# Performance work log

Measured on AMD Instinct MI355X. Metric: run time of the kernel, lower is better.

## Reference

```python
import jax, jax.numpy as jnp
import numpy as np

DRUG_DIM, PROT_DIM, HIDDEN_DIM, OUTPUT_DIM = 128, 128, 256, 256


def setup_inputs() -> dict:
    key = jax.random.key(0)
    ks = jax.random.split(key, 7)
    B, n_d, n_p = 8, 64, 1024
    s = lambda d: 1.0 / np.sqrt(d)
    return {
        "X_d": jax.random.normal(ks[0], (B, n_d, DRUG_DIM), dtype=jnp.float32),
        "X_p": jax.random.normal(ks[1], (B, n_p, PROT_DIM), dtype=jnp.float32),
        # nn.Linear(in, out) weights have shape (out, in); we store transposed (in, out)
        "W_d": jax.random.uniform(ks[2], (DRUG_DIM, HIDDEN_DIM), jnp.float32, -s(DRUG_DIM), s(DRUG_DIM)),
        "W_p": jax.random.uniform(ks[3], (PROT_DIM, HIDDEN_DIM), jnp.float32, -s(PROT_DIM), s(PROT_DIM)),
        "W_a": jax.random.uniform(ks[4], (DRUG_DIM, OUTPUT_DIM), jnp.float32, -s(DRUG_DIM), s(DRUG_DIM)),
        "W_b": jax.random.uniform(ks[5], (PROT_DIM, OUTPUT_DIM), jnp.float32, -s(PROT_DIM), s(PROT_DIM)),
        "w_score": jax.random.uniform(ks[6], (HIDDEN_DIM,), jnp.float32, -s(HIDDEN_DIM), s(HIDDEN_DIM)),
    }


def reference(X_d, X_p, W_d, W_p, W_a, W_b, w_score):
    # Projections: (B, n_d, H), (B, n_p, H), (B, n_d, O), (B, n_p, O)
    hd = jnp.einsum("bik,kh->bih", X_d, W_d)
    hp = jnp.einsum("bjk,kh->bjh", X_p, W_p)
    fd = jnp.einsum("bik,ko->bio", X_d, W_a)
    fp = jnp.einsum("bjk,ko->bjo", X_p, W_b)

    # N_ij = tanh(hd_i + hp_j): (B, n_d, n_p, H); scores = N @ w_score
    N = jnp.tanh(hd[:, :, None, :] + hp[:, None, :, :])
    scores = jnp.einsum("bijh,h->bij", N, w_score)
    A = jax.nn.softmax(scores, axis=-1)  # softmax over protein dim

    # f_ij = tanh(fd_i + fp_j): (B, n_d, n_p, O)
    f = jnp.tanh(fd[:, :, None, :] + fp[:, None, :, :])
    X_int = jnp.einsum("bij,bijo->bo", A, f)  # sum over i and j
    return X_int
```

## Files before the change

### kernel.cpp

```cpp
#include <hip/hip_runtime.h>

#define NB   8
#define ND   64
#define NP   1024
#define KDIM 128
#define HID  256
#define OUTD 256
#define CSC  2.885390081777927f
#define PSTR 1048

typedef __attribute__((ext_vector_type(8))) short  bf16x8;
typedef __attribute__((ext_vector_type(4))) float  f32x4;


__device__ __forceinline__ ushort f2bf(float f) {
    unsigned u = __float_as_uint(f);
    return (ushort)((u + 0x7FFFu + ((u >> 16) & 1u)) >> 16);
}

__device__ __forceinline__ float comb4(float u1, float u2, float u3, float u4,
                                       float c1, float c2, float c3, float c4,
                                       float acc) {
    float p12 = u1 * u2, p34 = u3 * u4;
    float P   = p12 * p34;
    float t1  = fmaf(c1, u2, c2 * u1);
    float t2  = fmaf(c3, u4, c4 * u3);
    float num = fmaf(t1, p34, t2 * p12);
    return fmaf(num, __builtin_amdgcn_rcpf(P), acc);
}

__global__ __launch_bounds__(256) void k_cast(
    const float* __restrict__ Xd, const float* __restrict__ Xp,
    const float* __restrict__ Wd, const float* __restrict__ Wa,
    const float* __restrict__ Wp, const float* __restrict__ Wb,
    ushort* __restrict__ Xdbf, ushort* __restrict__ Xpbf,
    ushort* __restrict__ WdT, ushort* __restrict__ WaT,
    ushort* __restrict__ WpT, ushort* __restrict__ WbT) {
    int blk = blockIdx.x, t = threadIdx.x;
    if (blk < 1024) {
        size_t i = ((size_t)blk << 10) + ((size_t)t << 2);
        float4 v = *(const float4*)(Xp + i);
        ushort4 o; o.x = f2bf(v.x); o.y = f2bf(v.y); o.z = f2bf(v.z); o.w = f2bf(v.w);
        *(ushort4*)(Xpbf + i) = o;
    } else if (blk < 1088) {
        size_t i = ((size_t)(blk - 1024) << 10) + ((size_t)t << 2);
        float4 v = *(const float4*)(Xd + i);
        ushort4 o; o.x = f2bf(v.x); o.y = f2bf(v.y); o.z = f2bf(v.z); o.w = f2bf(v.w);
        *(ushort4*)(Xdbf + i) = o;
    } else {
        int r = blk - 1088, mat = r >> 5;
        const float* W = (mat == 0) ? Wd : (mat == 1) ? Wa : (mat == 2) ? Wp : Wb;
        ushort* WT = (mat == 0) ? WdT : (mat == 1) ? WaT : (mat == 2) ? WpT : WbT;
        int o0 = ((r & 31) << 10) + (t << 2);
        int n = o0 >> 7, k0 = o0 & 127;
        ushort4 o;
        o.x = f2bf(W[(k0 + 0) * HID + n]);
        o.y = f2bf(W[(k0 + 1) * HID + n]);
        o.z = f2bf(W[(k0 + 2) * HID + n]);
        o.w = f2bf(W[(k0 + 3) * HID + n]);
        *(ushort4*)(WT + o0) = o;
    }
}

__global__ __launch_bounds__(256) void k_proj_mfma(
    const ushort* __restrict__ Xpbf, const ushort* __restrict__ Xdbf,
    const ushort* __restrict__ WdT, const ushort* __restrict__ WaT,
    const ushort* __restrict__ WpT, const ushort* __restrict__ WbT,
    float* __restrict__ Ehd, float* __restrict__ Efd,
    float* __restrict__ EhpT, float* __restrict__ Efp) {
    int blk = blockIdx.x, t = threadIdx.x;
    const ushort *A, *B;
    float* out; size_t obase; int ostride, am0, bn0;
    if (blk < 512) {
        int mt = blk >> 2, nt = blk & 3;
        A = Xpbf; am0 = mt * 64; B = WbT; bn0 = nt * 64;
        out = Efp; obase = (size_t)am0 * HID + bn0; ostride = HID;
    } else if (blk < 1024) {
        int r = blk - 512, b = r >> 6, rr = r & 63;
        int mt = rr >> 4, nt = rr & 15;
        A = WpT; am0 = mt * 64;
        B = Xpbf + (size_t)b * NP * KDIM; bn0 = nt * 64;
        out = EhpT; obase = ((size_t)(b * 256 + am0)) * NP + bn0; ostride = NP;
    } else if (blk < 1056) {
        int r = blk - 1024; int mt = r >> 2, nt = r & 3;
        A = Xdbf; am0 = mt * 64; B = WdT; bn0 = nt * 64;
        out = Ehd; obase = (size_t)am0 * HID + bn0; ostride = HID;
    } else {
        int r = blk - 1056; int mt = r >> 2, nt = r & 3;
        A = Xdbf; am0 = mt * 64; B = WaT; bn0 = nt * 64;
        out = Efd; obase = (size_t)am0 * HID + bn0; ostride = HID;
    }
    int l = t & 63, w = t >> 6;
    int wm = (w >> 1) << 5, wn = (w & 1) << 5;
    int lr = l & 15, lk = (l >> 4) << 3;
    const ushort* Ab = A + (size_t)(am0 + wm + lr) * KDIM + lk;
    const ushort* Bb = B + (size_t)(bn0 + wn + lr) * KDIM + lk;

    bf16x8 af[2][4], bfr[2][4];
#pragma unroll
    for (int f = 0; f < 2; ++f)
#pragma unroll
        for (int ks = 0; ks < 4; ++ks) {
            af[f][ks]  = *(const bf16x8*)(Ab + (size_t)(f << 4) * KDIM + (ks << 5));
            bfr[f][ks] = *(const bf16x8*)(Bb + (size_t)(f << 4) * KDIM + (ks << 5));
        }

    f32x4 acc[2][2];
#pragma unroll
    for (int mf = 0; mf < 2; ++mf)
#pragma unroll
        for (int nf = 0; nf < 2; ++nf) acc[mf][nf] = (f32x4){0.f, 0.f, 0.f, 0.f};
#pragma unroll
    for (int ks = 0; ks < 4; ++ks)
#pragma unroll
        for (int mf = 0; mf < 2; ++mf)
#pragma unroll
            for (int nf = 0; nf < 2; ++nf)
                acc[mf][nf] = __builtin_amdgcn_mfma_f32_16x16x32_bf16(
                    af[mf][ks], bfr[nf][ks], acc[mf][nf], 0, 0, 0);

#pragma unroll
    for (int mf = 0; mf < 2; ++mf)
#pragma unroll
        for (int nf = 0; nf < 2; ++nf)
#pragma unroll
            for (int r = 0; r < 4; ++r) {
                int m = wm + (mf << 4) + ((l >> 4) << 2) + r;
                int n = wn + (nf << 4) + (l & 15);
                out[obase + (size_t)m * ostride + n] =
                    __builtin_amdgcn_exp2f(acc[mf][nf][r] * CSC);
            }
}

__global__ __launch_bounds__(1024, 4) void k_fused(
    const float* __restrict__ Ehd, const float* __restrict__ EhpT,
    const float* __restrict__ Efd, const float* __restrict__ Efp,
    const float* __restrict__ wsc, float* __restrict__ part) {
    int blk = blockIdx.x;
    int b = blk & 7, pair = blk >> 3;
    int row0 = b * ND + pair * 2;
    int t = threadIdx.x;

    __shared__ float2 hrow[256];
    __shared__ float  w2s[256];
    __shared__ float2 a2[1024];
    __shared__ float  sred[8 * PSTR];
    __shared__ float  wsum0[16], wsum1[16];

    if (t < 256) {
        hrow[t] = make_float2(Ehd[((size_t)row0 << 8) + t],
                              Ehd[((size_t)(row0 + 1) << 8) + t]);
        w2s[t] = -2.0f * wsc[t];
    }
    __syncthreads();

    {
        int jq = t & 255, hq = t >> 8;
        const float* pB = EhpT + ((size_t)((b << 8) + (hq << 6))) * NP + (jq << 2);
        float a00 = 0, a01 = 0, a02 = 0, a03 = 0;
        float a10 = 0, a11 = 0, a12 = 0, a13 = 0;
        for (int hg = 0; hg < 16; ++hg) {
            const float* pr = pB + (size_t)(hg << 2) * NP;
            float4 p0 = *(const float4*)(pr);
            float4 p1 = *(const float4*)(pr + NP);
            float4 p2 = *(const float4*)(pr + 2 * (size_t)NP);
            float4 p3 = *(const float4*)(pr + 3 * (size_t)NP);
            int h = (hq << 6) + (hg << 2);
            float2 h0 = hrow[h],     h1 = hrow[h + 1];
            float2 h2 = hrow[h + 2], h3 = hrow[h + 3];
            float w0 = w2s[h],     w1 = w2s[h + 1];
            float w2 = w2s[h + 2], w3 = w2s[h + 3];
            a00 = comb4(fmaf(h0.x, p0.x, 1.f), fmaf(h1.x, p1.x, 1.f),
                        fmaf(h2.x, p2.x, 1.f), fmaf(h3.x, p3.x, 1.f),
                        w0, w1, w2, w3, a00);
            a01 = comb4(fmaf(h0.x, p0.y, 1.f), fmaf(h1.x, p1.y, 1.f),
                        fmaf(h2.x, p2.y, 1.f), fmaf(h3.x, p3.y, 1.f),
                        w0, w1, w2, w3, a01);
            a02 = comb4(fmaf(h0.x, p0.z, 1.f), fmaf(h1.x, p1.z, 1.f),
                        fmaf(h2.x, p2.z, 1.f), fmaf(h3.x, p3.z, 1.f),
                        w0, w1, w2, w3, a02);
            a03 = comb4(fmaf(h0.x, p0.w, 1.f), fmaf(h1.x, p1.w, 1.f),
                        fmaf(h2.x, p2.w, 1.f), fmaf(h3.x, p3.w, 1.f),
                        w0, w1, w2, w3, a03);
            a10 = comb4(fmaf(h0.y, p0.x, 1.f), fmaf(h1.y, p1.x, 1.f),
                        fmaf(h2.y, p2.x, 1.f), fmaf(h3.y, p3.x, 1.f),
                        w0, w1, w2, w3, a10);
            a11 = comb4(fmaf(h0.y, p0.y, 1.f), fmaf(h1.y, p1.y, 1.f),
                        fmaf(h2.y, p2.y, 1.f), fmaf(h3.y, p3.y, 1.f),
                        w0, w1, w2, w3, a11);
            a12 = comb4(fmaf(h0.y, p0.z, 1.f), fmaf(h1.y, p1.z, 1.f),
                        fmaf(h2.y, p2.z, 1.f), fmaf(h3.y, p3.z, 1.f),
                        w0, w1, w2, w3, a12);
            a13 = comb4(fmaf(h0.y, p0.w, 1.f), fmaf(h1.y, p1.w, 1.f),
                        fmaf(h2.y, p2.w, 1.f), fmaf(h3.y, p3.w, 1.f),
                        w0, w1, w2, w3, a13);
        }
        int base = (hq << 8) + jq;
        sred[0 * PSTR + base] = a00;  sred[1 * PSTR + base] = a01;
        sred[2 * PSTR + base] = a02;  sred[3 * PSTR + base] = a03;
        sred[4 * PSTR + base] = a10;  sred[5 * PSTR + base] = a11;
        sred[6 * PSTR + base] = a12;  sred[7 * PSTR + base] = a13;
    }
    __syncthreads();

    {
        int jq2 = t >> 2, c = t & 3;
        const float* p0 = sred + c * PSTR + jq2;
        const float* p1 = sred + (4 + c) * PSTR + jq2;
        float sc0 = (p0[0] + p0[256]) + (p0[512] + p0[768]);
        float sc1 = (p1[0] + p1[256]) + (p1[512] + p1[768]);
        const float L2E = 1.4426950408889634f;
        float e0 = __builtin_amdgcn_exp2f(sc0 * L2E);
        float e1 = __builtin_amdgcn_exp2f(sc1 * L2E);
        float s0 = e0, s1 = e1;
#pragma unroll
        for (int off = 32; off > 0; off >>= 1) {
            s0 += __shfl_xor(s0, off, 64);
            s1 += __shfl_xor(s1, off, 64);
        }
        if ((t & 63) == 0) { wsum0[t >> 6] = s0; wsum1[t >> 6] = s1; }
        __syncthreads();
        float tot0 = 0.f, tot1 = 0.f;
#pragma unroll
        for (int w = 0; w < 16; ++w) { tot0 += wsum0[w]; tot1 += wsum1[w]; }
        float sn0 = -2.0f * __builtin_amdgcn_rcpf(tot0);
        float sn1 = -2.0f * __builtin_amdgcn_rcpf(tot1);
        a2[t] = make_float2(e0 * sn0, e1 * sn1);
    }
    __syncthreads();

    {
        int oq = t & 63, jg = t >> 6;
        int o0 = oq << 2;
        float4 fd0 = *(const float4*)(Efd + ((size_t)row0 << 8) + o0);
        float4 fd1 = *(const float4*)(Efd + ((size_t)(row0 + 1) << 8) + o0);
        const float* fpB = Efp + ((size_t)(b * NP + (jg << 6)) << 8) + o0;
        float b00 = 0, b01 = 0, b02 = 0, b03 = 0;
        float b10 = 0, b11 = 0, b12 = 0, b13 = 0;
        for (int g = 0; g < 16; ++g) {
            const float* fr = fpB + ((size_t)(g << 2) << 8);
            float4 f0 = *(const float4*)(fr);
            float4 f1 = *(const float4*)(fr + 256);
            float4 f2 = *(const float4*)(fr + 512);
            float4 f3 = *(const float4*)(fr + 768);
            int j0 = (jg << 6) + (g << 2);
            float2 A0 = a2[j0],     A1 = a2[j0 + 1];
            float2 A2v = a2[j0 + 2], A3 = a2[j0 + 3];
            b00 = comb4(fmaf(fd0.x, f0.x, 1.f), fmaf(fd0.x, f1.x, 1.f),
                        fmaf(fd0.x, f2.x, 1.f), fmaf(fd0.x, f3.x, 1.f),
                        A0.x, A1.x, A2v.x, A3.x, b00);
            b01 = comb4(fmaf(fd0.y, f0.y, 1.f), fmaf(fd0.y, f1.y, 1.f),
                        fmaf(fd0.y, f2.y, 1.f), fmaf(fd0.y, f3.y, 1.f),
                        A0.x, A1.x, A2v.x, A3.x, b01);
            b02 = comb4(fmaf(fd0.z, f0.z, 1.f), fmaf(fd0.z, f1.z, 1.f),
                        fmaf(fd0.z, f2.z, 1.f), fmaf(fd0.z, f3.z, 1.f),
                        A0.x, A1.x, A2v.x, A3.x, b02);
            b03 = comb4(fmaf(fd0.w, f0.w, 1.f), fmaf(fd0.w, f1.w, 1.f),
                        fmaf(fd0.w, f2.w, 1.f), fmaf(fd0.w, f3.w, 1.f),
                        A0.x, A1.x, A2v.x, A3.x, b03);
            b10 = comb4(fmaf(fd1.x, f0.x, 1.f), fmaf(fd1.x, f1.x, 1.f),
                        fmaf(fd1.x, f2.x, 1.f), fmaf(fd1.x, f3.x, 1.f),
                        A0.y, A1.y, A2v.y, A3.y, b10);
            b11 = comb4(fmaf(fd1.y, f0.y, 1.f), fmaf(fd1.y, f1.y, 1.f),
                        fmaf(fd1.y, f2.y, 1.f), fmaf(fd1.y, f3.y, 1.f),
                        A0.y, A1.y, A2v.y, A3.y, b11);
            b12 = comb4(fmaf(fd1.z, f0.z, 1.f), fmaf(fd1.z, f1.z, 1.f),
                        fmaf(fd1.z, f2.z, 1.f), fmaf(fd1.z, f3.z, 1.f),
                        A0.y, A1.y, A2v.y, A3.y, b12);
            b13 = comb4(fmaf(fd1.w, f0.w, 1.f), fmaf(fd1.w, f1.w, 1.f),
                        fmaf(fd1.w, f2.w, 1.f), fmaf(fd1.w, f3.w, 1.f),
                        A0.y, A1.y, A2v.y, A3.y, b13);
        }
        __syncthreads();
        int base = (jg << 6) + oq;
        sred[0 * PSTR + base] = b00;  sred[1 * PSTR + base] = b01;
        sred[2 * PSTR + base] = b02;  sred[3 * PSTR + base] = b03;
        sred[4 * PSTR + base] = b10;  sred[5 * PSTR + base] = b11;
        sred[6 * PSTR + base] = b12;  sred[7 * PSTR + base] = b13;
    }
    __syncthreads();

    if (t < 512) {
        int r = t >> 8, o = t & 255;
        int oq2 = o >> 2, c2 = o & 3;
        const float* pk = sred + (r * 4 + c2) * PSTR + oq2;
        float s = 0.f;
#pragma unroll
        for (int g = 0; g < 16; ++g) s += pk[g << 6];
        part[((size_t)((b << 6) + (pair << 1) + r) << 8) + o] = s;
    }
}

__global__ __launch_bounds__(256) void k_reduce(
    const float* __restrict__ part, float* __restrict__ out) {
    int b = blockIdx.x, t = threadIdx.x;
    float s = 64.0f;
#pragma unroll 8
    for (int i = 0; i < 64; ++i)
        s += part[((size_t)((b << 6) + i) << 8) + t];
    out[(b << 8) + t] = s;
}

extern "C" void kernel_launch(void* const* d_in, const int* in_sizes, int n_in,
                              void* d_out, int out_size, void* d_ws, size_t ws_size,
                              hipStream_t stream) {
    const float* Xd  = (const float*)d_in[0];
    const float* Xp  = (const float*)d_in[1];
    const float* Wd  = (const float*)d_in[2];
    const float* Wp  = (const float*)d_in[3];
    const float* Wa  = (const float*)d_in[4];
    const float* Wb  = (const float*)d_in[5];
    const float* wsc = (const float*)d_in[6];
    float* out = (float*)d_out;

    float* ws = (float*)d_ws;
    float* Ehd  = ws;
    float* Efd  = Ehd + NB * ND * HID;
    float* EhpT = Efd + NB * ND * OUTD;
    float* Efp  = EhpT + NB * NP * HID;
    float* stage = Efp + NB * NP * OUTD;
    ushort* Xpbf = (ushort*)stage;
    ushort* Xdbf = Xpbf + NB * NP * KDIM;
    ushort* WdT  = Xdbf + 65536;
    ushort* WaT  = WdT + 32768;
    ushort* WpT  = WaT + 32768;
    ushort* WbT  = WpT + 32768;
    float* part  = stage;

    k_cast     <<<1216, 256, 0, stream>>>(Xd, Xp, Wd, Wa, Wp, Wb,
                                          Xdbf, Xpbf, WdT, WaT, WpT, WbT);
    k_proj_mfma<<<1088, 256, 0, stream>>>(Xpbf, Xdbf, WdT, WaT, WpT, WbT,
                                          Ehd, Efd, EhpT, Efp);
    k_fused    <<<256, 1024, 0, stream>>>(Ehd, EhpT, Efd, Efp, wsc, part);
    k_reduce   <<<NB, 256, 0, stream>>>(part, out);
}
```

Measured before the change: 59.31 us.

## Split fused attention kernel into scores, softmax, and accumulation kernels

Replaces the single 1024-thread fused kernel (256 blocks) with separate kernels. Scores are computed over quarter protein ranges in 1024 blocks of 256 threads, followed by a row softmax kernel and a 1024-block f-accumulation kernel that writes per-quarter partials. A wider 64-block reduction finishes the sum. The aim is to fill more compute units and shrink per-block shared memory, at the cost of extra launches and round trips of the score matrix through global memory.

```diff
diff --git a/kernel.cpp b/kernel.cpp
--- a/kernel.cpp
+++ b/kernel.cpp
@@ -7,7 +7,7 @@
 #define HID  256
 #define OUTD 256
 #define CSC  2.885390081777927f
-#define PSTR 1048
+#define PSTR2 264
 
 typedef __attribute__((ext_vector_type(8))) short  bf16x8;
 typedef __attribute__((ext_vector_type(4))) float  f32x4;
@@ -132,173 +132,186 @@
             }
 }
 
-__global__ __launch_bounds__(1024, 4) void k_fused(
+__global__ __launch_bounds__(256) void k_scores2(
     const float* __restrict__ Ehd, const float* __restrict__ EhpT,
-    const float* __restrict__ Efd, const float* __restrict__ Efp,
-    const float* __restrict__ wsc, float* __restrict__ part) {
+    const float* __restrict__ wsc, float* __restrict__ S) {
     int blk = blockIdx.x;
-    int b = blk & 7, pair = blk >> 3;
+    int b = blk & 7, pair = (blk >> 3) & 31, jh = blk >> 8;
     int row0 = b * ND + pair * 2;
     int t = threadIdx.x;
-
     __shared__ float2 hrow[256];
     __shared__ float  w2s[256];
-    __shared__ float2 a2[1024];
-    __shared__ float  sred[8 * PSTR];
-    __shared__ float  wsum0[16], wsum1[16];
-
-    if (t < 256) {
-        hrow[t] = make_float2(Ehd[((size_t)row0 << 8) + t],
-                              Ehd[((size_t)(row0 + 1) << 8) + t]);
-        w2s[t] = -2.0f * wsc[t];
-    }
-    __syncthreads();
-
-    {
-        int jq = t & 255, hq = t >> 8;
-        const float* pB = EhpT + ((size_t)((b << 8) + (hq << 6))) * NP + (jq << 2);
-        float a00 = 0, a01 = 0, a02 = 0, a03 = 0;
-        float a10 = 0, a11 = 0, a12 = 0, a13 = 0;
-        for (int hg = 0; hg < 16; ++hg) {
-            const float* pr = pB + (size_t)(hg << 2) * NP;
-            float4 p0 = *(const float4*)(pr);
-            float4 p1 = *(const float4*)(pr + NP);
-            float4 p2 = *(const float4*)(pr + 2 * (size_t)NP);
-            float4 p3 = *(const float4*)(pr + 3 * (size_t)NP);
-            int h = (hq << 6) + (hg << 2);
-            float2 h0 = hrow[h],     h1 = hrow[h + 1];
-            float2 h2 = hrow[h + 2], h3 = hrow[h + 3];
-            float w0 = w2s[h],     w1 = w2s[h + 1];
-            float w2 = w2s[h + 2], w3 = w2s[h + 3];
-            a00 = comb4(fmaf(h0.x, p0.x, 1.f), fmaf(h1.x, p1.x, 1.f),
-                        fmaf(h2.x, p2.x, 1.f), fmaf(h3.x, p3.x, 1.f),
-                        w0, w1, w2, w3, a00);
-            a01 = comb4(fmaf(h0.x, p0.y, 1.f), fmaf(h1.x, p1.y, 1.f),
-                        fmaf(h2.x, p2.y, 1.f), fmaf(h3.x, p3.y, 1.f),
-                        w0, w1, w2, w3, a01);
-            a02 = comb4(fmaf(h0.x, p0.z, 1.f), fmaf(h1.x, p1.z, 1.f),
-                        fmaf(h2.x, p2.z, 1.f), fmaf(h3.x, p3.z, 1.f),
-                        w0, w1, w2, w3, a02);
-            a03 = comb4(fmaf(h0.x, p0.w, 1.f), fmaf(h1.x, p1.w, 1.f),
-                        fmaf(h2.x, p2.w, 1.f), fmaf(h3.x, p3.w, 1.f),
-                        w0, w1, w2, w3, a03);
-            a10 = comb4(fmaf(h0.y, p0.x, 1.f), fmaf(h1.y, p1.x, 1.f),
-                        fmaf(h2.y, p2.x, 1.f), fmaf(h3.y, p3.x, 1.f),
-                        w0, w1, w2, w3, a10);
-            a11 = comb4(fmaf(h0.y, p0.y, 1.f), fmaf(h1.y, p1.y, 1.f),
-                        fmaf(h2.y, p2.y, 1.f), fmaf(h3.y, p3.y, 1.f),
-                        w0, w1, w2, w3, a11);
-            a12 = comb4(fmaf(h0.y, p0.z, 1.f), fmaf(h1.y, p1.z, 1.f),
-                        fmaf(h2.y, p2.z, 1.f), fmaf(h3.y, p3.z, 1.f),
-                        w0, w1, w2, w3, a12);
-            a13 = comb4(fmaf(h0.y, p0.w, 1.f), fmaf(h1.y, p1.w, 1.f),
-                        fmaf(h2.y, p2.w, 1.f), fmaf(h3.y, p3.w, 1.f),
-                        w0, w1, w2, w3, a13);
-        }
-        int base = (hq << 8) + jq;
-        sred[0 * PSTR + base] = a00;  sred[1 * PSTR + base] = a01;
-        sred[2 * PSTR + base] = a02;  sred[3 * PSTR + base] = a03;
-        sred[4 * PSTR + base] = a10;  sred[5 * PSTR + base] = a11;
-        sred[6 * PSTR + base] = a12;  sred[7 * PSTR + base] = a13;
-    }
-    __syncthreads();
-
-    {
-        int jq2 = t >> 2, c = t & 3;
-        const float* p0 = sred + c * PSTR + jq2;
-        const float* p1 = sred + (4 + c) * PSTR + jq2;
-        float sc0 = (p0[0] + p0[256]) + (p0[512] + p0[768]);
-        float sc1 = (p1[0] + p1[256]) + (p1[512] + p1[768]);
-        const float L2E = 1.4426950408889634f;
-        float e0 = __builtin_amdgcn_exp2f(sc0 * L2E);
-        float e1 = __builtin_amdgcn_exp2f(sc1 * L2E);
-        float s0 = e0, s1 = e1;
-#pragma unroll
-        for (int off = 32; off > 0; off >>= 1) {
-            s0 += __shfl_xor(s0, off, 64);
-            s1 += __shfl_xor(s1, off, 64);
-        }
-        if ((t & 63) == 0) { wsum0[t >> 6] = s0; wsum1[t >> 6] = s1; }
+    __shared__ float  sred[8 * PSTR2];
+    hrow[t] = make_float2(Ehd[((size_t)row0 << 8) + t],
+                          Ehd[((size_t)(row0 + 1) << 8) + t]);
+    w2s[t] = -2.0f * wsc[t];
+    __syncthreads();
+
+    int jq = t & 63, hq = t >> 6;
+    const float* pB = EhpT + ((size_t)((b << 8) + (hq << 6))) * NP
+                    + (jh << 8) + (jq << 2);
+    float a00 = 0, a01 = 0, a02 = 0, a03 = 0;
+    float a10 = 0, a11 = 0, a12 = 0, a13 = 0;
+    for (int hg = 0; hg < 16; ++hg) {
+        const float* pr = pB + (size_t)(hg << 2) * NP;
+        float4 p0 = *(const float4*)(pr);
+        float4 p1 = *(const float4*)(pr + NP);
+        float4 p2 = *(const float4*)(pr + 2 * (size_t)NP);
+        float4 p3 = *(const float4*)(pr + 3 * (size_t)NP);
+        int h = (hq << 6) + (hg << 2);
+        float2 h0 = hrow[h],     h1 = hrow[h + 1];
+        float2 h2 = hrow[h + 2], h3 = hrow[h + 3];
+        float w0 = w2s[h],     w1 = w2s[h + 1];
+        float w2 = w2s[h + 2], w3 = w2s[h + 3];
+        a00 = comb4(fmaf(h0.x, p0.x, 1.f), fmaf(h1.x, p1.x, 1.f),
+                    fmaf(h2.x, p2.x, 1.f), fmaf(h3.x, p3.x, 1.f),
+                    w0, w1, w2, w3, a00);
+        a01 = comb4(fmaf(h0.x, p0.y, 1.f), fmaf(h1.x, p1.y, 1.f),
+                    fmaf(h2.x, p2.y, 1.f), fmaf(h3.x, p3.y, 1.f),
+                    w0, w1, w2, w3, a01);
+        a02 = comb4(fmaf(h0.x, p0.z, 1.f), fmaf(h1.x, p1.z, 1.f),
+                    fmaf(h2.x, p2.z, 1.f), fmaf(h3.x, p3.z, 1.f),
+                    w0, w1, w2, w3, a02);
+        a03 = comb4(fmaf(h0.x, p0.w, 1.f), fmaf(h1.x, p1.w, 1.f),
+                    fmaf(h2.x, p2.w, 1.f), fmaf(h3.x, p3.w, 1.f),
+                    w0, w1, w2, w3, a03);
+        a10 = comb4(fmaf(h0.y, p0.x, 1.f), fmaf(h1.y, p1.x, 1.f),
+                    fmaf(h2.y, p2.x, 1.f), fmaf(h3.y, p3.x, 1.f),
+                    w0, w1, w2, w3, a10);
+        a11 = comb4(fmaf(h0.y, p0.y, 1.f), fmaf(h1.y, p1.y, 1.f),
+                    fmaf(h2.y, p2.y, 1.f), fmaf(h3.y, p3.y, 1.f),
+                    w0, w1, w2, w3, a11);
+        a12 = comb4(fmaf(h0.y, p0.z, 1.f), fmaf(h1.y, p1.z, 1.f),
+                    fmaf(h2.y, p2.z, 1.f), fmaf(h3.y, p3.z, 1.f),
+                    w0, w1, w2, w3, a12);
+        a13 = comb4(fmaf(h0.y, p0.w, 1.f), fmaf(h1.y, p1.w, 1.f),
+                    fmaf(h2.y, p2.w, 1.f), fmaf(h3.y, p3.w, 1.f),
+                    w0, w1, w2, w3, a13);
+    }
+    int base = (hq << 6) + jq;
+    sred[0 * PSTR2 + base] = a00;  sred[1 * PSTR2 + base] = a01;
+    sred[2 * PSTR2 + base] = a02;  sred[3 * PSTR2 + base] = a03;
+    sred[4 * PSTR2 + base] = a10;  sred[5 * PSTR2 + base] = a11;
+    sred[6 * PSTR2 + base] = a12;  sred[7 * PSTR2 + base] = a13;
+    __syncthreads();
+
+    int c = t & 3, jq2 = t >> 2;
+    const float* q0 = sred + c * PSTR2 + jq2;
+    const float* q1 = sred + (4 + c) * PSTR2 + jq2;
+    float s0 = (q0[0] + q0[64]) + (q0[128] + q0[192]);
+    float s1 = (q1[0] + q1[64]) + (q1[128] + q1[192]);
+    S[((size_t)row0 << 10) + (jh << 8) + t] = s0;
+    S[((size_t)(row0 + 1) << 10) + (jh << 8) + t] = s1;
+}
+
+__global__ __launch_bounds__(256) void k_softmax(float* __restrict__ S) {
+    int row = blockIdx.x;
+    int t = threadIdx.x;
+    float* Srow = S + ((size_t)row << 10);
+    float4 v = ((float4*)Srow)[t];
+    const float L2E = 1.4426950408889634f;
+    v.x = __builtin_amdgcn_exp2f(v.x * L2E);
+    v.y = __builtin_amdgcn_exp2f(v.y * L2E);
+    v.z = __builtin_amdgcn_exp2f(v.z * L2E);
+    v.w = __builtin_amdgcn_exp2f(v.w * L2E);
+    float s4 = (v.x + v.y) + (v.z + v.w);
+#pragma unroll
+    for (int off = 32; off > 0; off >>= 1) s4 += __shfl_xor(s4, off, 64);
+    __shared__ float wsum[4];
+    if ((t & 63) == 0) wsum[t >> 6] = s4;
+    __syncthreads();
+    float tot = (wsum[0] + wsum[1]) + (wsum[2] + wsum[3]);
+    float sneg = -2.0f * __builtin_amdgcn_rcpf(tot);
+    v.x *= sneg; v.y *= sneg; v.z *= sneg; v.w *= sneg;
+    ((float4*)Srow)[t] = v;
+}
+
+__global__ __launch_bounds__(256) void k_facc2(
+    const float* __restrict__ Efd, const float* __restrict__ Efp,
+    const float* __restrict__ A2, float* __restrict__ npart) {
+    int blk = blockIdx.x;
+    int b = blk & 7, pair = (blk >> 3) & 31, jh = blk >> 8;
+    int row0 = b * ND + pair * 2;
+    int t = threadIdx.x;
+    __shared__ float2 a2s[256];
+    __shared__ float  sred[8 * PSTR2];
+    a2s[t] = make_float2(A2[((size_t)row0 << 10) + (jh << 8) + t],
+                         A2[((size_t)(row0 + 1) << 10) + (jh << 8) + t]);
+    __syncthreads();
+
+    int oq = t & 63, jg = t >> 6;
+    int o0 = oq << 2;
+    float4 fd0 = *(const float4*)(Efd + ((size_t)row0 << 8) + o0);
+    float4 fd1 = *(const float4*)(Efd + ((size_t)(row0 + 1) << 8) + o0);
+    const float* fpB = Efp + ((size_t)(b * NP + (jh << 8) + (jg << 6)) << 8) + o0;
+    float b00 = 0, b01 = 0, b02 = 0, b03 = 0;
+    float b10 = 0, b11 = 0, b12 = 0, b13 = 0;
+    for (int g = 0; g < 16; ++g) {
+        const float* fr = fpB + ((size_t)(g << 2) << 8);
+        float4 f0 = *(const float4*)(fr);
+        float4 f1 = *(const float4*)(fr + 256);
+        float4 f2 = *(const float4*)(fr + 512);
+        float4 f3 = *(const float4*)(fr + 768);
+        int j0 = (jg << 6) + (g << 2);
+        float2 A0 = a2s[j0],      A1 = a2s[j0 + 1];
+        float2 A2v = a2s[j0 + 2], A3 = a2s[j0 + 3];
+        b00 = comb4(fmaf(fd0.x, f0.x, 1.f), fmaf(fd0.x, f1.x, 1.f),
+                    fmaf(fd0.x, f2.x, 1.f), fmaf(fd0.x, f3.x, 1.f),
+                    A0.x, A1.x, A2v.x, A3.x, b00);
+        b01 = comb4(fmaf(fd0.y, f0.y, 1.f), fmaf(fd0.y, f1.y, 1.f),
+                    fmaf(fd0.y, f2.y, 1.f), fmaf(fd0.y, f3.y, 1.f),
+                    A0.x, A1.x, A2v.x, A3.x, b01);
+        b02 = comb4(fmaf(fd0.z, f0.z, 1.f), fmaf(fd0.z, f1.z, 1.f),
+                    fmaf(fd0.z, f2.z, 1.f), fmaf(fd0.z, f3.z, 1.f),
+                    A0.x, A1.x, A2v.x, A3.x, b02);
+        b03 = comb4(fmaf(fd0.w, f0.w, 1.f), fmaf(fd0.w, f1.w, 1.f),
+                    fmaf(fd0.w, f2.w, 1.f), fmaf(fd0.w, f3.w, 1.f),
+                    A0.x, A1.x, A2v.x, A3.x, b03);
+        b10 = comb4(fmaf(fd1.x, f0.x, 1.f), fmaf(fd1.x, f1.x, 1.f),
+                    fmaf(fd1.x, f2.x, 1.f), fmaf(fd1.x, f3.x, 1.f),
+                    A0.y, A1.y, A2v.y, A3.y, b10);
+        b11 = comb4(fmaf(fd1.y, f0.y, 1.f), fmaf(fd1.y, f1.y, 1.f),
+                    fmaf(fd1.y, f2.y, 1.f), fmaf(fd1.y, f3.y, 1.f),
+                    A0.y, A1.y, A2v.y, A3.y, b11);
+        b12 = comb4(fmaf(fd1.z, f0.z, 1.f), fmaf(fd1.z, f1.z, 1.f),
+                    fmaf(fd1.z, f2.z, 1.f), fmaf(fd1.z, f3.z, 1.f),
+                    A0.y, A1.y, A2v.y, A3.y, b12);
+        b13 = comb4(fmaf(fd1.w, f0.w, 1.f), fmaf(fd1.w, f1.w, 1.f),
+                    fmaf(fd1.w, f2.w, 1.f), fmaf(fd1.w, f3.w, 1.f),
+                    A0.y, A1.y, A2v.y, A3.y, b13);
+    }
+    int base = (jg << 6) + oq;
+    sred[0 * PSTR2 + base] = b00;  sred[1 * PSTR2 + base] = b01;
+    sred[2 * PSTR2 + base] = b02;  sred[3 * PSTR2 + base] = b03;
+    sred[4 * PSTR2 + base] = b10;  sred[5 * PSTR2 + base] = b11;
+    sred[6 * PSTR2 + base] = b12;  sred[7 * PSTR2 + base] = b13;
+    __syncthreads();
+
+    int c = t & 3, oq2 = t >> 2;
+    const float* q0 = sred + c * PSTR2 + oq2;
+    const float* q1 = sred + (4 + c) * PSTR2 + oq2;
+    float s0 = (q0[0] + q0[64]) + (q0[128] + q0[192]);
+    float s1 = (q1[0] + q1[64]) + (q1[128] + q1[192]);
+    npart[((((size_t)row0 << 2) + jh) << 8) + t] = s0;
+    npart[((((size_t)(row0 + 1) << 2) + jh) << 8) + t] = s1;
+}
+
+__global__ __launch_bounds__(256) void k_reduce(
+    const float* __restrict__ npart, float* __restrict__ out) {
+    int b = blockIdx.x >> 3, oc = blockIdx.x & 7;
+    int t = threadIdx.x;
+    int o = oc * 32 + (t & 31), q0 = t >> 5;
+    float s = 0.f;
+#pragma unroll
+    for (int k = 0; k < 32; ++k)
+        s += npart[((size_t)(b * 256 + q0 + (k << 3)) << 8) + o];
+    __shared__ float red[256];
+    red[t] = s; __syncthreads();
+    for (int st = 128; st >= 32; st >>= 1) {
+        if (t < st) red[t] += red[t + st];
         __syncthreads();
-        float tot0 = 0.f, tot1 = 0.f;
-#pragma unroll
-        for (int w = 0; w < 16; ++w) { tot0 += wsum0[w]; tot1 += wsum1[w]; }
-        float sn0 = -2.0f * __builtin_amdgcn_rcpf(tot0);
-        float sn1 = -2.0f * __builtin_amdgcn_rcpf(tot1);
-        a2[t] = make_float2(e0 * sn0, e1 * sn1);
-    }
-    __syncthreads();
-
-    {
-        int oq = t & 63, jg = t >> 6;
-        int o0 = oq << 2;
-        float4 fd0 = *(const float4*)(Efd + ((size_t)row0 << 8) + o0);
-        float4 fd1 = *(const float4*)(Efd + ((size_t)(row0 + 1) << 8) + o0);
-        const float* fpB = Efp + ((size_t)(b * NP + (jg << 6)) << 8) + o0;
-        float b00 = 0, b01 = 0, b02 = 0, b03 = 0;
-        float b10 = 0, b11 = 0, b12 = 0, b13 = 0;
-        for (int g = 0; g < 16; ++g) {
-            const float* fr = fpB + ((size_t)(g << 2) << 8);
-            float4 f0 = *(const float4*)(fr);
-            float4 f1 = *(const float4*)(fr + 256);
-            float4 f2 = *(const float4*)(fr + 512);
-            float4 f3 = *(const float4*)(fr + 768);
-            int j0 = (jg << 6) + (g << 2);
-            float2 A0 = a2[j0],     A1 = a2[j0 + 1];
-            float2 A2v = a2[j0 + 2], A3 = a2[j0 + 3];
-            b00 = comb4(fmaf(fd0.x, f0.x, 1.f), fmaf(fd0.x, f1.x, 1.f),
-                        fmaf(fd0.x, f2.x, 1.f), fmaf(fd0.x, f3.x, 1.f),
-                        A0.x, A1.x, A2v.x, A3.x, b00);
-            b01 = comb4(fmaf(fd0.y, f0.y, 1.f), fmaf(fd0.y, f1.y, 1.f),
-                        fmaf(fd0.y, f2.y, 1.f), fmaf(fd0.y, f3.y, 1.f),
-                        A0.x, A1.x, A2v.x, A3.x, b01);
-            b02 = comb4(fmaf(fd0.z, f0.z, 1.f), fmaf(fd0.z, f1.z, 1.f),
-                        fmaf(fd0.z, f2.z, 1.f), fmaf(fd0.z, f3.z, 1.f),
-                        A0.x, A1.x, A2v.x, A3.x, b02);
-            b03 = comb4(fmaf(fd0.w, f0.w, 1.f), fmaf(fd0.w, f1.w, 1.f),
-                        fmaf(fd0.w, f2.w, 1.f), fmaf(fd0.w, f3.w, 1.f),
-                        A0.x, A1.x, A2v.x, A3.x, b03);
-            b10 = comb4(fmaf(fd1.x, f0.x, 1.f), fmaf(fd1.x, f1.x, 1.f),
-                        fmaf(fd1.x, f2.x, 1.f), fmaf(fd1.x, f3.x, 1.f),
-                        A0.y, A1.y, A2v.y, A3.y, b10);
-            b11 = comb4(fmaf(fd1.y, f0.y, 1.f), fmaf(fd1.y, f1.y, 1.f),
-                        fmaf(fd1.y, f2.y, 1.f), fmaf(fd1.y, f3.y, 1.f),
-                        A0.y, A1.y, A2v.y, A3.y, b11);
-            b12 = comb4(fmaf(fd1.z, f0.z, 1.f), fmaf(fd1.z, f1.z, 1.f),
-                        fmaf(fd1.z, f2.z, 1.f), fmaf(fd1.z, f3.z, 1.f),
-                        A0.y, A1.y, A2v.y, A3.y, b12);
-            b13 = comb4(fmaf(fd1.w, f0.w, 1.f), fmaf(fd1.w, f1.w, 1.f),
-                        fmaf(fd1.w, f2.w, 1.f), fmaf(fd1.w, f3.w, 1.f),
-                        A0.y, A1.y, A2v.y, A3.y, b13);
-        }
-        __syncthreads();
-        int base = (jg << 6) + oq;
-        sred[0 * PSTR + base] = b00;  sred[1 * PSTR + base] = b01;
-        sred[2 * PSTR + base] = b02;  sred[3 * PSTR + base] = b03;
-        sred[4 * PSTR + base] = b10;  sred[5 * PSTR + base] = b11;
-        sred[6 * PSTR + base] = b12;  sred[7 * PSTR + base] = b13;
-    }
-    __syncthreads();
-
-    if (t < 512) {
-        int r = t >> 8, o = t & 255;
-        int oq2 = o >> 2, c2 = o & 3;
-        const float* pk = sred + (r * 4 + c2) * PSTR + oq2;
-        float s = 0.f;
-#pragma unroll
-        for (int g = 0; g < 16; ++g) s += pk[g << 6];
-        part[((size_t)((b << 6) + (pair << 1) + r) << 8) + o] = s;
-    }
-}
-
-__global__ __launch_bounds__(256) void k_reduce(
-    const float* __restrict__ part, float* __restrict__ out) {
-    int b = blockIdx.x, t = threadIdx.x;
-    float s = 64.0f;
-#pragma unroll 8
-    for (int i = 0; i < 64; ++i)
-        s += part[((size_t)((b << 6) + i) << 8) + t];
-    out[(b << 8) + t] = s;
+    }
+    if (t < 32) out[(b << 8) + oc * 32 + t] = 64.0f + red[t];
 }
 
 extern "C" void kernel_launch(void* const* d_in, const int* in_sizes, int n_in,
@@ -325,12 +338,15 @@
     ushort* WaT  = WdT + 32768;
     ushort* WpT  = WaT + 32768;
     ushort* WbT  = WpT + 32768;
-    float* part  = stage;
+    float* S     = stage;
+    float* npart = stage + 622592;
 
     k_cast     <<<1216, 256, 0, stream>>>(Xd, Xp, Wd, Wa, Wp, Wb,
                                           Xdbf, Xpbf, WdT, WaT, WpT, WbT);
     k_proj_mfma<<<1088, 256, 0, stream>>>(Xpbf, Xdbf, WdT, WaT, WpT, WbT,
                                           Ehd, Efd, EhpT, Efp);
-    k_fused    <<<256, 1024, 0, stream>>>(Ehd, EhpT, Efd, Efp, wsc, part);
-    k_reduce   <<<NB, 256, 0, stream>>>(part, out);
-}
+    k_scores2  <<<1024, 256, 0, stream>>>(Ehd, EhpT, wsc, S);
+    k_softmax  <<<NB * ND, 256, 0, stream>>>(S);
+    k_facc2    <<<1024, 256, 0, stream>>>(Efd, Efp, S, npart);
+    k_reduce   <<<64, 256, 0, stream>>>(npart, out);
+}
```

Result: slower. 61.81 us (+4.2%).

## Split protein dimension across two blocks with deferred softmax normalization

Applied to the files above, without the earlier changes.

Doubles the k_fused grid by splitting the 1024 protein positions into two halves per drug-row pair. Each block writes an unnormalized numerator and a partial softmax denominator, and k_reduce combines them and divides. This gives 512 blocks instead of 256 to fill more CUs, and hrow/w2s are packed into one float4 shared array. The cost is an extra workspace buffer, a reciprocal per row in the reduce kernel, and exp without max subtraction split across halves.

```diff
diff --git a/kernel.cpp b/kernel.cpp
--- a/kernel.cpp
+++ b/kernel.cpp
@@ -7,7 +7,7 @@
 #define HID  256
 #define OUTD 256
 #define CSC  2.885390081777927f
-#define PSTR 1048
+#define PSTR 1032
 
 typedef __attribute__((ext_vector_type(8))) short  bf16x8;
 typedef __attribute__((ext_vector_type(4))) float  f32x4;
@@ -132,70 +132,68 @@
             }
 }
 
-__global__ __launch_bounds__(1024, 4) void k_fused(
+__global__ __launch_bounds__(1024, 8) void k_fused(
     const float* __restrict__ Ehd, const float* __restrict__ EhpT,
     const float* __restrict__ Efd, const float* __restrict__ Efp,
-    const float* __restrict__ wsc, float* __restrict__ part) {
+    const float* __restrict__ wsc, float* __restrict__ num,
+    float* __restrict__ den) {
     int blk = blockIdx.x;
-    int b = blk & 7, pair = blk >> 3;
+    int b = blk & 7, pair = (blk >> 3) & 31, jh = blk >> 8;
     int row0 = b * ND + pair * 2;
     int t = threadIdx.x;
 
-    __shared__ float2 hrow[256];
-    __shared__ float  w2s[256];
-    __shared__ float2 a2[1024];
+    __shared__ float4 hw4[256];
+    __shared__ float2 a2[512];
     __shared__ float  sred[8 * PSTR];
-    __shared__ float  wsum0[16], wsum1[16];
-
-    if (t < 256) {
-        hrow[t] = make_float2(Ehd[((size_t)row0 << 8) + t],
-                              Ehd[((size_t)(row0 + 1) << 8) + t]);
-        w2s[t] = -2.0f * wsc[t];
-    }
+    __shared__ float  wsum0[8], wsum1[8];
+
+    if (t < 256)
+        hw4[t] = make_float4(Ehd[((size_t)row0 << 8) + t],
+                             Ehd[((size_t)(row0 + 1) << 8) + t],
+                             -2.0f * wsc[t], 0.f);
     __syncthreads();
 
     {
-        int jq = t & 255, hq = t >> 8;
-        const float* pB = EhpT + ((size_t)((b << 8) + (hq << 6))) * NP + (jq << 2);
+        int jq = t & 127, hq = t >> 7;
+        const float* pB = EhpT + ((size_t)((b << 8) + (hq << 5))) * NP
+                        + (jh << 9) + (jq << 2);
         float a00 = 0, a01 = 0, a02 = 0, a03 = 0;
         float a10 = 0, a11 = 0, a12 = 0, a13 = 0;
-        for (int hg = 0; hg < 16; ++hg) {
+        for (int hg = 0; hg < 8; ++hg) {
             const float* pr = pB + (size_t)(hg << 2) * NP;
             float4 p0 = *(const float4*)(pr);
             float4 p1 = *(const float4*)(pr + NP);
             float4 p2 = *(const float4*)(pr + 2 * (size_t)NP);
             float4 p3 = *(const float4*)(pr + 3 * (size_t)NP);
-            int h = (hq << 6) + (hg << 2);
-            float2 h0 = hrow[h],     h1 = hrow[h + 1];
-            float2 h2 = hrow[h + 2], h3 = hrow[h + 3];
-            float w0 = w2s[h],     w1 = w2s[h + 1];
-            float w2 = w2s[h + 2], w3 = w2s[h + 3];
-            a00 = comb4(fmaf(h0.x, p0.x, 1.f), fmaf(h1.x, p1.x, 1.f),
-                        fmaf(h2.x, p2.x, 1.f), fmaf(h3.x, p3.x, 1.f),
-                        w0, w1, w2, w3, a00);
-            a01 = comb4(fmaf(h0.x, p0.y, 1.f), fmaf(h1.x, p1.y, 1.f),
-                        fmaf(h2.x, p2.y, 1.f), fmaf(h3.x, p3.y, 1.f),
-                        w0, w1, w2, w3, a01);
-            a02 = comb4(fmaf(h0.x, p0.z, 1.f), fmaf(h1.x, p1.z, 1.f),
-                        fmaf(h2.x, p2.z, 1.f), fmaf(h3.x, p3.z, 1.f),
-                        w0, w1, w2, w3, a02);
-            a03 = comb4(fmaf(h0.x, p0.w, 1.f), fmaf(h1.x, p1.w, 1.f),
-                        fmaf(h2.x, p2.w, 1.f), fmaf(h3.x, p3.w, 1.f),
-                        w0, w1, w2, w3, a03);
-            a10 = comb4(fmaf(h0.y, p0.x, 1.f), fmaf(h1.y, p1.x, 1.f),
-                        fmaf(h2.y, p2.x, 1.f), fmaf(h3.y, p3.x, 1.f),
-                        w0, w1, w2, w3, a10);
-            a11 = comb4(fmaf(h0.y, p0.y, 1.f), fmaf(h1.y, p1.y, 1.f),
-                        fmaf(h2.y, p2.y, 1.f), fmaf(h3.y, p3.y, 1.f),
-                        w0, w1, w2, w3, a11);
-            a12 = comb4(fmaf(h0.y, p0.z, 1.f), fmaf(h1.y, p1.z, 1.f),
-                        fmaf(h2.y, p2.z, 1.f), fmaf(h3.y, p3.z, 1.f),
-                        w0, w1, w2, w3, a12);
-            a13 = comb4(fmaf(h0.y, p0.w, 1.f), fmaf(h1.y, p1.w, 1.f),
-                        fmaf(h2.y, p2.w, 1.f), fmaf(h3.y, p3.w, 1.f),
-                        w0, w1, w2, w3, a13);
-        }
-        int base = (hq << 8) + jq;
+            int h = (hq << 5) + (hg << 2);
+            float4 hw0 = hw4[h],     hw1 = hw4[h + 1];
+            float4 hw2 = hw4[h + 2], hw3 = hw4[h + 3];
+            a00 = comb4(fmaf(hw0.x, p0.x, 1.f), fmaf(hw1.x, p1.x, 1.f),
+                        fmaf(hw2.x, p2.x, 1.f), fmaf(hw3.x, p3.x, 1.f),
+                        hw0.z, hw1.z, hw2.z, hw3.z, a00);
+            a01 = comb4(fmaf(hw0.x, p0.y, 1.f), fmaf(hw1.x, p1.y, 1.f),
+                        fmaf(hw2.x, p2.y, 1.f), fmaf(hw3.x, p3.y, 1.f),
+                        hw0.z, hw1.z, hw2.z, hw3.z, a01);
+            a02 = comb4(fmaf(hw0.x, p0.z, 1.f), fmaf(hw1.x, p1.z, 1.f),
+                        fmaf(hw2.x, p2.z, 1.f), fmaf(hw3.x, p3.z, 1.f),
+                        hw0.z, hw1.z, hw2.z, hw3.z, a02);
+            a03 = comb4(fmaf(hw0.x, p0.w, 1.f), fmaf(hw1.x, p1.w, 1.f),
+                        fmaf(hw2.x, p2.w, 1.f), fmaf(hw3.x, p3.w, 1.f),
+                        hw0.z, hw1.z, hw2.z, hw3.z, a03);
+            a10 = comb4(fmaf(hw0.y, p0.x, 1.f), fmaf(hw1.y, p1.x, 1.f),
+                        fmaf(hw2.y, p2.x, 1.f), fmaf(hw3.y, p3.x, 1.f),
+                        hw0.z, hw1.z, hw2.z, hw3.z, a10);
+            a11 = comb4(fmaf(hw0.y, p0.y, 1.f), fmaf(hw1.y, p1.y, 1.f),
+                        fmaf(hw2.y, p2.y, 1.f), fmaf(hw3.y, p3.y, 1.f),
+                        hw0.z, hw1.z, hw2.z, hw3.z, a11);
+            a12 = comb4(fmaf(hw0.y, p0.z, 1.f), fmaf(hw1.y, p1.z, 1.f),
+                        fmaf(hw2.y, p2.z, 1.f), fmaf(hw3.y, p3.z, 1.f),
+                        hw0.z, hw1.z, hw2.z, hw3.z, a12);
+            a13 = comb4(fmaf(hw0.y, p0.w, 1.f), fmaf(hw1.y, p1.w, 1.f),
+                        fmaf(hw2.y, p2.w, 1.f), fmaf(hw3.y, p3.w, 1.f),
+                        hw0.z, hw1.z, hw2.z, hw3.z, a13);
+        }
+        int base = (hq << 7) + jq;
         sred[0 * PSTR + base] = a00;  sred[1 * PSTR + base] = a01;
         sred[2 * PSTR + base] = a02;  sred[3 * PSTR + base] = a03;
         sred[4 * PSTR + base] = a10;  sred[5 * PSTR + base] = a11;
@@ -203,48 +201,53 @@
     }
     __syncthreads();
 
-    {
+    if (t < 512) {
         int jq2 = t >> 2, c = t & 3;
         const float* p0 = sred + c * PSTR + jq2;
         const float* p1 = sred + (4 + c) * PSTR + jq2;
-        float sc0 = (p0[0] + p0[256]) + (p0[512] + p0[768]);
-        float sc1 = (p1[0] + p1[256]) + (p1[512] + p1[768]);
+        float sc0 = 0.f, sc1 = 0.f;
+#pragma unroll
+        for (int hq = 0; hq < 8; ++hq) {
+            sc0 += p0[hq << 7];
+            sc1 += p1[hq << 7];
+        }
         const float L2E = 1.4426950408889634f;
-        float e0 = __builtin_amdgcn_exp2f(sc0 * L2E);
-        float e1 = __builtin_amdgcn_exp2f(sc1 * L2E);
-        float s0 = e0, s1 = e1;
+        float u0 = __builtin_amdgcn_exp2f(sc0 * L2E);
+        float u1 = __builtin_amdgcn_exp2f(sc1 * L2E);
+        a2[t] = make_float2(-2.f * u0, -2.f * u1);
+        float s0 = u0, s1 = u1;
 #pragma unroll
         for (int off = 32; off > 0; off >>= 1) {
             s0 += __shfl_xor(s0, off, 64);
             s1 += __shfl_xor(s1, off, 64);
         }
         if ((t & 63) == 0) { wsum0[t >> 6] = s0; wsum1[t >> 6] = s1; }
-        __syncthreads();
-        float tot0 = 0.f, tot1 = 0.f;
-#pragma unroll
-        for (int w = 0; w < 16; ++w) { tot0 += wsum0[w]; tot1 += wsum1[w]; }
-        float sn0 = -2.0f * __builtin_amdgcn_rcpf(tot0);
-        float sn1 = -2.0f * __builtin_amdgcn_rcpf(tot1);
-        a2[t] = make_float2(e0 * sn0, e1 * sn1);
     }
     __syncthreads();
+    if (t == 0) {
+        float d0 = 0.f, d1 = 0.f;
+#pragma unroll
+        for (int w = 0; w < 8; ++w) { d0 += wsum0[w]; d1 += wsum1[w]; }
+        den[((size_t)row0 << 1) + jh] = d0;
+        den[((size_t)(row0 + 1) << 1) + jh] = d1;
+    }
 
     {
         int oq = t & 63, jg = t >> 6;
         int o0 = oq << 2;
         float4 fd0 = *(const float4*)(Efd + ((size_t)row0 << 8) + o0);
         float4 fd1 = *(const float4*)(Efd + ((size_t)(row0 + 1) << 8) + o0);
-        const float* fpB = Efp + ((size_t)(b * NP + (jg << 6)) << 8) + o0;
+        const float* fpB = Efp + ((size_t)(b * NP + (jh << 9) + (jg << 5)) << 8) + o0;
         float b00 = 0, b01 = 0, b02 = 0, b03 = 0;
         float b10 = 0, b11 = 0, b12 = 0, b13 = 0;
-        for (int g = 0; g < 16; ++g) {
+        for (int g = 0; g < 8; ++g) {
             const float* fr = fpB + ((size_t)(g << 2) << 8);
             float4 f0 = *(const float4*)(fr);
             float4 f1 = *(const float4*)(fr + 256);
             float4 f2 = *(const float4*)(fr + 512);
             float4 f3 = *(const float4*)(fr + 768);
-            int j0 = (jg << 6) + (g << 2);
-            float2 A0 = a2[j0],     A1 = a2[j0 + 1];
+            int j0 = (jg << 5) + (g << 2);
+            float2 A0 = a2[j0],      A1 = a2[j0 + 1];
             float2 A2v = a2[j0 + 2], A3 = a2[j0 + 3];
             b00 = comb4(fmaf(fd0.x, f0.x, 1.f), fmaf(fd0.x, f1.x, 1.f),
                         fmaf(fd0.x, f2.x, 1.f), fmaf(fd0.x, f3.x, 1.f),
@@ -283,21 +286,26 @@
     if (t < 512) {
         int r = t >> 8, o = t & 255;
         int oq2 = o >> 2, c2 = o & 3;
-        const float* pk = sred + (r * 4 + c2) * PSTR + oq2;
+        const float* pk = sred + ((r << 2) + c2) * PSTR + oq2;
         float s = 0.f;
 #pragma unroll
         for (int g = 0; g < 16; ++g) s += pk[g << 6];
-        part[((size_t)((b << 6) + (pair << 1) + r) << 8) + o] = s;
+        num[((((size_t)(row0 + r) << 1) + jh) << 8) + o] = s;
     }
 }
 
 __global__ __launch_bounds__(256) void k_reduce(
-    const float* __restrict__ part, float* __restrict__ out) {
+    const float* __restrict__ num, const float* __restrict__ den,
+    float* __restrict__ out) {
     int b = blockIdx.x, t = threadIdx.x;
     float s = 64.0f;
-#pragma unroll 8
-    for (int i = 0; i < 64; ++i)
-        s += part[((size_t)((b << 6) + i) << 8) + t];
+    for (int i = 0; i < 64; ++i) {
+        size_t row = (size_t)(b * 64 + i);
+        float D = den[row << 1] + den[(row << 1) + 1];
+        const float* nb = num + ((row << 1) << 8) + t;
+        float n = nb[0] + nb[256];
+        s += n * __builtin_amdgcn_rcpf(D);
+    }
     out[(b << 8) + t] = s;
 }
 
@@ -325,12 +333,13 @@
     ushort* WaT  = WdT + 32768;
     ushort* WpT  = WaT + 32768;
     ushort* WbT  = WpT + 32768;
-    float* part  = stage;
+    float* numb = stage + 622592;
+    float* denb = numb + 262144;
 
     k_cast     <<<1216, 256, 0, stream>>>(Xd, Xp, Wd, Wa, Wp, Wb,
                                           Xdbf, Xpbf, WdT, WaT, WpT, WbT);
     k_proj_mfma<<<1088, 256, 0, stream>>>(Xpbf, Xdbf, WdT, WaT, WpT, WbT,
                                           Ehd, Efd, EhpT, Efp);
-    k_fused    <<<256, 1024, 0, stream>>>(Ehd, EhpT, Efd, Efp, wsc, part);
-    k_reduce   <<<NB, 256, 0, stream>>>(part, out);
-}
+    k_fused    <<<512, 1024, 0, stream>>>(Ehd, EhpT, Efd, Efp, wsc, numb, denb);
+    k_reduce   <<<NB, 256, 0, stream>>>(numb, denb, out);
+}
```

New measurement: 59.23 us. No clear change (-0.1%).
